# Performance work log

Hardware: AMD Instinct MI355X
Metric: run time of the kernel (lower is better)

## Reference

```python
import jax, jax.numpy as jnp
import numpy as np

PSEUDO3D = True
DO_TUBE = True
DILATION_ITERATIONS = 1

# Neighbor offsets P2..P9 (clockwise from north), as in Zhang-Suen / skimage skeletonize
_OFFS = [(-1, 0), (-1, 1), (0, 1), (1, 1), (1, 0), (1, -1), (0, -1), (-1, -1)]


def _shift(a, dy, dx):
    # out[n, y, x] = a[n, y+dy, x+dx], zero-padded borders (same as skimage's 0-pad)
    N, H, W = a.shape
    p = jnp.pad(a, ((0, 0), (1, 1), (1, 1)))
    return p[:, 1 + dy:1 + dy + H, 1 + dx:1 + dx + W]


def _subiter(img, first):
    # One Zhang-Suen sub-iteration on a stack of 2D slices [N, H, W] (bool)
    P = [_shift(img, dy, dx) for dy, dx in _OFFS]
    B = sum(p.astype(jnp.int32) for p in P)            # nonzero-neighbor count
    seq = P + [P[0]]
    A = sum(((~seq[k]) & seq[k + 1]).astype(jnp.int32) for k in range(8))  # 0->1 transitions
    P2, P3, P4, P5, P6, P7, P8, P9 = P
    if first:
        c = (~(P2 & P4 & P6)) & (~(P4 & P6 & P8))
    else:
        c = (~(P2 & P4 & P8)) & (~(P2 & P6 & P8))
    remove = img & (B >= 2) & (B <= 6) & (A == 1) & c
    return img & ~remove


def _thin_stack(stack):
    # Zhang-Suen thinning of every 2D slice in a [N, H, W] bool stack, run to convergence.
    # All slices are processed in one while_loop; converged slices are fixed points, so
    # extra iterations are no-ops and the result matches per-slice skeletonize.
    def body(state):
        img, _ = state
        new = _subiter(_subiter(img, True), False)
        return new, jnp.any(new != img)

    def cond(state):
        return state[1]

    img, _ = jax.lax.while_loop(cond, body, (stack, jnp.array(True)))
    return img


def _dilate6(v):
    # scipy.ndimage.binary_dilation with the default 6-connected 3D structure, border 0
    D, H, W = v.shape
    p = jnp.pad(v, 1)
    out = v
    for dz, dy, dx in [(1, 0, 0), (-1, 0, 0), (0, 1, 0), (0, -1, 0), (0, 0, 1), (0, 0, -1)]:
        out = out | p[1 + dz:1 + dz + D, 1 + dy:1 + dy + H, 1 + dx:1 + dx + W]
    return out


def setup_inputs() -> dict:
    key = jax.random.key(0)
    gt = jax.random.randint(key, (1, 48, 384, 384), 0, 2).astype(jnp.float32)
    return {"gt_skel": gt}


def reference(gt_skel):
    vol = gt_skel[0]                      # squeeze(axis=0) -> [D, H, W]
    mask = vol == 1.0                     # bool
    skel = _thin_stack(mask)              # per z-slice skeletonize
    if PSEUDO3D:
        # per y-slice: mask[:, y, :] has shape [D, W]
        skel = skel | jnp.transpose(_thin_stack(jnp.transpose(mask, (1, 0, 2))), (1, 0, 2))
        # per x-slice: mask[:, :, x] has shape [D, H]
        skel = skel | jnp.transpose(_thin_stack(jnp.transpose(mask, (2, 0, 1))), (1, 2, 0))
    if DO_TUBE:
        for _ in range(DILATION_ITERATIONS):
            skel = _dilate6(skel)
    skel = skel & mask                    # skel &= gt_skel.astype(bool) (values are 0/1)
    return skel[None].astype(jnp.float32)
```

## Files before the change

### kernel.cpp

```cpp
#include <hip/hip_runtime.h>

typedef unsigned long long u64;

constexpr int D = 48, H = 384, W = 384;
constexpr int WPR = 6;
constexpr int PADW = 8;
constexpr int NVOX = D * H * W;
constexpr int NWVOL = D * H * WPR;
constexpr int MPAD2 = 52;
constexpr int NXY = (D + 2) * PADW;
constexpr int NTILE = D * 36;

__device__ __forceinline__ void fa(u64 a, u64 b, u64 c, u64& s, u64& cy) {
  u64 x = a ^ b;
  s = x ^ c;
  cy = (a & b) | (c & x);
}

__device__ __forceinline__ u64 zs_regs(u64 w00, u64 w01, u64 w02,
                                       u64 w10, u64 w11, u64 w12,
                                       u64 w20, u64 w21, u64 w22, bool first) {
  const u64 P2 = w01;
  const u64 P3 = (w01 >> 1) | (w02 << 63);
  const u64 P4 = (w11 >> 1) | (w12 << 63);
  const u64 P5 = (w21 >> 1) | (w22 << 63);
  const u64 P6 = w21;
  const u64 P7 = (w21 << 1) | (w20 >> 63);
  const u64 P8 = (w11 << 1) | (w10 >> 63);
  const u64 P9 = (w01 << 1) | (w00 >> 63);

  u64 s1, c1, s2, c2, s3, c3, u0, u1, v1, v2;
  fa(P2, P3, P4, s1, c1);
  fa(P5, P6, P7, s2, c2);
  fa(P8, P9, 0ull, s3, c3);
  fa(s1, s2, s3, u0, u1);
  fa(c1, c2, c3, v1, v2);
  u64 b1 = u1 ^ v1, k2 = u1 & v1;
  u64 b2 = v2 ^ k2, b3 = v2 & k2;
  u64 condB = (b1 | b2 | b3) & ~(b3 | (b2 & b1 & u0));

  u64 t0 = ~P2 & P3, t1 = ~P3 & P4, t2 = ~P4 & P5, t3 = ~P5 & P6;
  u64 t4 = ~P6 & P7, t5 = ~P7 & P8, t6 = ~P8 & P9, t7 = ~P9 & P2;
  fa(t0, t1, t2, s1, c1);
  fa(t3, t4, t5, s2, c2);
  fa(t6, t7, 0ull, s3, c3);
  fa(s1, s2, s3, u0, u1);
  fa(c1, c2, c3, v1, v2);
  u64 a1 = u1 ^ v1, j2 = u1 & v1;
  u64 a2 = v2 ^ j2, a3 = v2 & j2;
  u64 condA = u0 & ~(a1 | a2 | a3);

  u64 cc = first ? ((~(P2 & P4 & P6)) & (~(P4 & P6 & P8)))
                 : ((~(P2 & P4 & P8)) & (~(P2 & P6 & P8)));
  return w11 & ~(condB & condA & cc);
}

__device__ __forceinline__ u64 dirty_wave(const u64* __restrict__ U, int mw) {
  const u64 A = U[mw - 1], B = U[mw], C = U[mw + 1], Dw = U[mw + 2];
  const u64 smA = A | (A >> 1 | B << 63) | (A >> 2 | B << 62);
  const u64 smB = B | (B >> 1 | C << 63) | (B >> 2 | C << 62);
  const u64 smC = C | (C >> 1 | Dw << 63) | (C >> 2 | Dw << 62);
  const u64 Dm9 = (smB << 9) | (smA >> 55);
  const u64 Dm1 = (smB << 1) | (smA >> 63);
  const u64 Dp7 = (smB >> 7) | (smC << 57);
  return Dm9 | Dm1 | Dp7;
}

template<int R, bool FIRST>
__device__ __forceinline__ void subpass(const u64* __restrict__ src, u64* __restrict__ dst,
                                        u64* rawW, const u64* rawPrev,
                                        u64* Uw, const u64* Ur,
                                        int* chgflag, int tid, int nthr) {
  constexpr int NP = (R + 2) * PADW;
  int anych = 0;
  for (int base = 0; base < NP; base += nthr) {
    const int idx = base + tid;
    int changed = 0;
    if (idx < NP) {
      const int mw = 1 + (idx >> 6);
      const u64 dmask = dirty_wave(Ur, mw);
      if ((dmask >> (idx & 63)) & 1ull) {
        const u64 old = src[idx];
        u64 nw = 0;
        if (old) {
          nw = zs_regs(src[idx - PADW - 1], src[idx - PADW], src[idx - PADW + 1],
                       src[idx - 1], old, src[idx + 1],
                       src[idx + PADW - 1], src[idx + PADW], src[idx + PADW + 1], FIRST);
          changed = (nw != old);
        }
        dst[idx] = nw;
        anych |= changed;
      }
    }
    const u64 bal = __ballot(changed != 0);
    if ((tid & 63) == 0 && idx < NP) {
      const int mw = 1 + (idx >> 6);
      rawW[mw] = bal;
      Uw[mw] = bal | rawPrev[mw];
    }
  }
  if (anych) *chgflag = 1;
}

template<bool FIRST>
__device__ __forceinline__ void xy_dense(const u64* __restrict__ src, u64* __restrict__ dst,
                                         int* chgflag, int tid) {
  int anych = 0;
  if (tid < NXY) {
    const u64 old = src[tid];
    u64 nw = 0;
    if (old) {
      nw = zs_regs(src[tid - PADW - 1], src[tid - PADW], src[tid - PADW + 1],
                   src[tid - 1], old, src[tid + 1],
                   src[tid + PADW - 1], src[tid + PADW], src[tid + PADW + 1], FIRST);
      anych = (nw != old);
    }
    dst[tid] = nw;
  }
  if (anych) *chgflag = 1;
}

template<int R>
__device__ __forceinline__ void thin_z(const u64* __restrict__ maskP,
                                       u64* __restrict__ skelZ,
                                       int slice, u64* Abuf, u64* Bbuf,
                                       u64 (*raw)[MPAD2], u64 (*Um)[MPAD2],
                                       int* s_chg) {
  constexpr int NP = (R + 2) * PADW;
  constexpr int MW = (NP + 63) >> 6;
  const int tid = threadIdx.x;
  const int nthr = 1024;

  for (int idx = tid; idx < NP; idx += nthr) {
    const int rp = idx >> 3, cp = idx & 7;
    u64 v = 0;
    if (rp >= 1 && rp <= R && cp >= 1 && cp <= 6)
      v = maskP[(slice * H + (rp - 1)) * WPR + (cp - 1)];
    Abuf[idx] = v;
    Bbuf[idx] = 0;
  }
  for (int t = tid; t < 4 * MPAD2; t += nthr) {
    const int arr = t / MPAD2, j = t - arr * MPAD2;
    const u64 v = ((arr & 1) && j >= 1 && j <= MW) ? ~0ull : 0ull;
    if (arr < 2) raw[arr][j] = v; else Um[arr - 2][j] = v;
  }
  if (tid < 2) s_chg[tid] = 0;
  __syncthreads();

  int k = 0;
  while (true) {
    subpass<R, true >(Abuf, Bbuf, raw[0], raw[1], Um[0], Um[1], &s_chg[k], tid, nthr);
    __syncthreads();
    if (tid == 0) s_chg[k ^ 1] = 0;
    subpass<R, false>(Bbuf, Abuf, raw[1], raw[0], Um[1], Um[0], &s_chg[k], tid, nthr);
    __syncthreads();
    if (s_chg[k] == 0) break;
    k ^= 1;
  }

  for (int idx = tid; idx < NP; idx += nthr) {
    const int rp = idx >> 3, cp = idx & 7;
    if (rp < 1 || rp > R || cp < 1 || cp > 6) continue;
    skelZ[(slice * H + (rp - 1)) * WPR + (cp - 1)] = Abuf[idx];
  }
}

template<int MODE>
__device__ __forceinline__ void thin_xy(const u64* __restrict__ maskP,
                                        u64* __restrict__ dstBuf,
                                        int slice, u64* Abuf, u64* Bbuf,
                                        int* s_chg) {
  const int tid = threadIdx.x;

  if (MODE == 1) {
    if (tid < NXY) {
      const int rp = tid >> 3, cp = tid & 7;
      u64 v = 0;
      if (rp >= 1 && rp <= D && cp >= 1 && cp <= 6)
        v = maskP[((rp - 1) * H + slice) * WPR + (cp - 1)];
      Abuf[tid] = v;
      Bbuf[tid] = 0;
    }
  } else {
    const int lane = tid & 63, wave = tid >> 6;
    const int xw = slice >> 6, xb = slice & 63;
    for (int w = wave; w < NXY; w += 16) {
      const int rp = w >> 3, cp = w & 7;
      u64 val = 0;
      if (rp >= 1 && rp <= D && cp >= 1 && cp <= 6) {
        const int c = (cp - 1) * 64 + lane;
        u64 bit = (maskP[((rp - 1) * H + c) * WPR + xw] >> xb) & 1ull;
        val = __ballot(bit != 0);
      }
      if (lane == 0) { Abuf[w] = val; Bbuf[w] = 0; }
    }
  }
  if (tid < 2) s_chg[tid] = 0;
  __syncthreads();

  int k = 0;
  while (true) {
    xy_dense<true >(Abuf, Bbuf, &s_chg[k], tid);
    __syncthreads();
    if (tid == 0) s_chg[k ^ 1] = 0;
    xy_dense<false>(Bbuf, Abuf, &s_chg[k], tid);
    __syncthreads();
    if (s_chg[k] == 0) break;
    k ^= 1;
  }

  if (tid < NXY) {
    const int rp = tid >> 3, cp = tid & 7;
    if (rp >= 1 && rp <= D && cp >= 1 && cp <= 6) {
      const u64 w = Abuf[tid];
      if (MODE == 1) dstBuf[((rp - 1) * H + slice) * WPR + (cp - 1)] = w;
      else           dstBuf[((rp - 1) * W + slice) * WPR + (cp - 1)] = w;
    }
  }
}

__global__ __launch_bounds__(1024) void thin_all(const u64* __restrict__ maskP,
                                                 u64* __restrict__ skelZ,
                                                 u64* __restrict__ skelY,
                                                 u64* __restrict__ skelX) {
  __shared__ u64 Abuf[(H + 2) * PADW];
  __shared__ u64 Bbuf[(H + 2) * PADW];
  __shared__ u64 raw[2][MPAD2];
  __shared__ u64 Um[2][MPAD2];
  __shared__ int s_chg[2];
  const int b = blockIdx.x;
  if (b < D) {
    thin_z<H>(maskP, skelZ, b, Abuf, Bbuf, raw, Um, s_chg);
  } else if (b < D + H) {
    thin_xy<1>(maskP, skelY, b - D, Abuf, Bbuf, s_chg);
  } else {
    thin_xy<2>(maskP, skelX, b - D - H, Abuf, Bbuf, s_chg);
  }
}

__global__ void init_pack(const float* __restrict__ in, u64* __restrict__ maskP) {
  const int lane = threadIdx.x & 63;
  const int gwave = (blockIdx.x * blockDim.x + threadIdx.x) >> 6;
  const int nwaves = (gridDim.x * blockDim.x) >> 6;
  for (int widx = gwave; widx < NWVOL; widx += nwaves) {
    float v = in[(size_t)widx * 64 + lane];
    u64 w = __ballot(v == 1.0f);
    if (lane == 0) maskP[widx] = w;
  }
}

__global__ void transpose_x(const u64* __restrict__ skelX,
                            u64* __restrict__ skelXT) {
  const int gw = (blockIdx.x * blockDim.x + threadIdx.x) >> 6;
  const int lane = threadIdx.x & 63;
  const int z = gw / 36, rem = gw - z * 36;
  const int yw = rem / 6, xw = rem - yw * 6;
  const int x = xw * 64 + lane;
  const u64 wx = skelX[(z * W + x) * WPR + yw];
  u64 mine = 0;
  #pragma unroll 8
  for (int j = 0; j < 64; ++j) {
    u64 wj = __ballot((wx >> j) & 1ull);
    if (lane == j) mine = wj;
  }
  const int y = yw * 64 + lane;
  skelXT[(z * H + y) * WPR + xw] = mine;
}

__global__ __launch_bounds__(256) void dilate_expand(const u64* __restrict__ maskP,
                                                     const u64* __restrict__ sZ,
                                                     const u64* __restrict__ sY,
                                                     const u64* __restrict__ sXT,
                                                     float* __restrict__ out) {
  __shared__ u64 rw[64];
  const int tid = threadIdx.x;
  const int wbase = blockIdx.x * 64;
  if (tid < 64) {
    const int wi = wbase + tid;
    const int wc = wi % WPR;
    const int row = wi / WPR;
    const int y = row % H;
    const int z = row / H;
    const u64 S = sZ[wi] | sY[wi] | sXT[wi];
    const u64 L = (wc > 0) ? (sZ[wi - 1] | sY[wi - 1] | sXT[wi - 1]) : 0ull;
    const u64 Rw = (wc < WPR - 1) ? (sZ[wi + 1] | sY[wi + 1] | sXT[wi + 1]) : 0ull;
    u64 d = S | (S << 1) | (L >> 63) | (S >> 1) | (Rw << 63);
    if (y > 0)     d |= sZ[wi - WPR] | sY[wi - WPR] | sXT[wi - WPR];
    if (y < H - 1) d |= sZ[wi + WPR] | sY[wi + WPR] | sXT[wi + WPR];
    if (z > 0)     d |= sZ[wi - H * WPR] | sY[wi - H * WPR] | sXT[wi - H * WPR];
    if (z < D - 1) d |= sZ[wi + H * WPR] | sY[wi + H * WPR] | sXT[wi + H * WPR];
    rw[tid] = d & maskP[wi];
  }
  __syncthreads();
  float4* o4 = reinterpret_cast<float4*>(out + (size_t)wbase * 64);
  #pragma unroll
  for (int k = 0; k < 4; ++k) {
    const int f = tid + 256 * k;
    const u64 bits = rw[f >> 4] >> ((f & 15) * 4);
    float4 o;
    o.x = (float)(bits & 1ull);
    o.y = (float)((bits >> 1) & 1ull);
    o.z = (float)((bits >> 2) & 1ull);
    o.w = (float)((bits >> 3) & 1ull);
    o4[f] = o;
  }
}

extern "C" void kernel_launch(void* const* d_in, const int* in_sizes, int n_in,
                              void* d_out, int out_size, void* d_ws, size_t ws_size,
                              hipStream_t stream) {
  const float* in = (const float*)d_in[0];
  float* out = (float*)d_out;
  u64* wsw = (u64*)d_ws;
  u64* maskP = wsw;
  u64* skelZ = wsw + NWVOL;
  u64* skelY = wsw + 2 * NWVOL;
  u64* skelX = wsw + 3 * NWVOL;
  u64* skelXT = wsw + 4 * NWVOL;

  init_pack<<<1728, 256, 0, stream>>>(in, maskP);
  thin_all<<<D + H + W, 1024, 0, stream>>>(maskP, skelZ, skelY, skelX);
  transpose_x<<<(NTILE * 64) / 256, 256, 0, stream>>>(skelX, skelXT);
  dilate_expand<<<NWVOL / 64, 256, 0, stream>>>(maskP, skelZ, skelY, skelXT, out);
}
```

Measured before the change: 61.97 us.

## Split early z-slice thinning into haloed row bands and fuse transpose

The first 16 Zhang-Suen sub-passes of each z-slice now run in four row bands per slice, each with a 16-row halo. Because one sub-pass can only change pixels one row away, the central band rows match the global result exactly. A second kernel loads that partial state per full slice and iterates to convergence, and the leftover blocks of that kernel also do the x-skeleton bit transpose, which removes a separate launch. The aim is to spread the long serial z-slice work over more blocks early on, since 48 slice blocks were likely the critical path. The cost is redundant halo computation, an extra global round trip through curZ, and the dirty-tracking masks being reset to full at the start of the finish phase.

```diff
diff --git a/kernel.cpp b/kernel.cpp
--- a/kernel.cpp
+++ b/kernel.cpp
@@ -10,6 +10,12 @@
 constexpr int MPAD2 = 52;
 constexpr int NXY = (D + 2) * PADW;
 constexpr int NTILE = D * 36;
+
+constexpr int BAND = 96;
+constexpr int HALO = 16;
+constexpr int KA = 16;
+constexpr int BROWS = BAND + 2 * HALO;
+constexpr int NBAND = H / BAND;
 
 __device__ __forceinline__ void fa(u64 a, u64 b, u64 c, u64& s, u64& cy) {
   u64 x = a ^ b;
@@ -70,10 +76,10 @@
 __device__ __forceinline__ void subpass(const u64* __restrict__ src, u64* __restrict__ dst,
                                         u64* rawW, const u64* rawPrev,
                                         u64* Uw, const u64* Ur,
-                                        int* chgflag, int tid, int nthr) {
+                                        int* chgflag, int tid) {
   constexpr int NP = (R + 2) * PADW;
   int anych = 0;
-  for (int base = 0; base < NP; base += nthr) {
+  for (int base = 0; base < NP; base += 1024) {
     const int idx = base + tid;
     int changed = 0;
     if (idx < NP) {
@@ -102,6 +108,15 @@
   if (anych) *chgflag = 1;
 }
 
+template<int MW>
+__device__ __forceinline__ void init_masks(u64 (*raw)[MPAD2], u64 (*Um)[MPAD2], int tid) {
+  for (int t = tid; t < 4 * MPAD2; t += 1024) {
+    const int arr = t / MPAD2, j = t - arr * MPAD2;
+    const u64 v = ((arr & 1) && j >= 1 && j <= MW) ? ~0ull : 0ull;
+    if (arr < 2) raw[arr][j] = v; else Um[arr - 2][j] = v;
+  }
+}
+
 template<bool FIRST>
 __device__ __forceinline__ void xy_dense(const u64* __restrict__ src, u64* __restrict__ dst,
                                          int* chgflag, int tid) {
@@ -120,48 +135,42 @@
   if (anych) *chgflag = 1;
 }
 
-template<int R>
-__device__ __forceinline__ void thin_z(const u64* __restrict__ maskP,
-                                       u64* __restrict__ skelZ,
-                                       int slice, u64* Abuf, u64* Bbuf,
-                                       u64 (*raw)[MPAD2], u64 (*Um)[MPAD2],
-                                       int* s_chg) {
-  constexpr int NP = (R + 2) * PADW;
+__device__ __forceinline__ void band_body(const u64* __restrict__ maskP,
+                                          u64* __restrict__ curZ,
+                                          int zi, int band, u64* Abuf, u64* Bbuf,
+                                          u64 (*raw)[MPAD2], u64 (*Um)[MPAD2],
+                                          int* s_chg) {
+  constexpr int NP = (BROWS + 2) * PADW;
   constexpr int MW = (NP + 63) >> 6;
   const int tid = threadIdx.x;
-  const int nthr = 1024;
-
-  for (int idx = tid; idx < NP; idx += nthr) {
+  const int g0 = band * BAND - HALO;
+
+  for (int idx = tid; idx < NP; idx += 1024) {
     const int rp = idx >> 3, cp = idx & 7;
+    const int g = g0 + rp - 1;
     u64 v = 0;
-    if (rp >= 1 && rp <= R && cp >= 1 && cp <= 6)
-      v = maskP[(slice * H + (rp - 1)) * WPR + (cp - 1)];
+    if (rp >= 1 && rp <= BROWS && cp >= 1 && cp <= 6 && g >= 0 && g < H)
+      v = maskP[(zi * H + g) * WPR + (cp - 1)];
     Abuf[idx] = v;
     Bbuf[idx] = 0;
   }
-  for (int t = tid; t < 4 * MPAD2; t += nthr) {
-    const int arr = t / MPAD2, j = t - arr * MPAD2;
-    const u64 v = ((arr & 1) && j >= 1 && j <= MW) ? ~0ull : 0ull;
-    if (arr < 2) raw[arr][j] = v; else Um[arr - 2][j] = v;
-  }
-  if (tid < 2) s_chg[tid] = 0;
+  init_masks<MW>(raw, Um, tid);
+  if (tid == 0) s_chg[0] = 0;
   __syncthreads();
 
-  int k = 0;
-  while (true) {
-    subpass<R, true >(Abuf, Bbuf, raw[0], raw[1], Um[0], Um[1], &s_chg[k], tid, nthr);
-    __syncthreads();
-    if (tid == 0) s_chg[k ^ 1] = 0;
-    subpass<R, false>(Bbuf, Abuf, raw[1], raw[0], Um[1], Um[0], &s_chg[k], tid, nthr);
-    __syncthreads();
-    if (s_chg[k] == 0) break;
-    k ^= 1;
-  }
-
-  for (int idx = tid; idx < NP; idx += nthr) {
+  for (int t = 0; t < KA; t += 2) {
+    subpass<BROWS, true >(Abuf, Bbuf, raw[0], raw[1], Um[0], Um[1], &s_chg[0], tid);
+    __syncthreads();
+    subpass<BROWS, false>(Bbuf, Abuf, raw[1], raw[0], Um[1], Um[0], &s_chg[0], tid);
+    __syncthreads();
+  }
+
+  for (int idx = tid; idx < NP; idx += 1024) {
     const int rp = idx >> 3, cp = idx & 7;
-    if (rp < 1 || rp > R || cp < 1 || cp > 6) continue;
-    skelZ[(slice * H + (rp - 1)) * WPR + (cp - 1)] = Abuf[idx];
+    if (rp < 1 || rp > BROWS || cp < 1 || cp > 6) continue;
+    const int g = g0 + rp - 1;
+    if (g < band * BAND || g >= band * BAND + BAND) continue;
+    curZ[(zi * H + g) * WPR + (cp - 1)] = Abuf[idx];
   }
 }
 
@@ -219,22 +228,85 @@
   }
 }
 
-__global__ __launch_bounds__(1024) void thin_all(const u64* __restrict__ maskP,
-                                                 u64* __restrict__ skelZ,
-                                                 u64* __restrict__ skelY,
-                                                 u64* __restrict__ skelX) {
+__global__ __launch_bounds__(1024) void thin_bands_xy(const u64* __restrict__ maskP,
+                                                      u64* __restrict__ skelY,
+                                                      u64* __restrict__ skelX,
+                                                      u64* __restrict__ curZ) {
+  __shared__ u64 Abuf[(BROWS + 2) * PADW];
+  __shared__ u64 Bbuf[(BROWS + 2) * PADW];
+  __shared__ u64 raw[2][MPAD2];
+  __shared__ u64 Um[2][MPAD2];
+  __shared__ int s_chg[2];
+  const int b = blockIdx.x;
+  if (b < D * NBAND) {
+    band_body(maskP, curZ, b >> 2, b & 3, Abuf, Bbuf, raw, Um, s_chg);
+  } else {
+    const int q = b - D * NBAND;
+    if (q < H) thin_xy<1>(maskP, skelY, q, Abuf, Bbuf, s_chg);
+    else       thin_xy<2>(maskP, skelX, q - H, Abuf, Bbuf, s_chg);
+  }
+}
+
+__global__ __launch_bounds__(1024) void thin_z_finish(const u64* __restrict__ curZ,
+                                                      u64* __restrict__ skelZ,
+                                                      const u64* __restrict__ skelX,
+                                                      u64* __restrict__ skelXT) {
   __shared__ u64 Abuf[(H + 2) * PADW];
   __shared__ u64 Bbuf[(H + 2) * PADW];
   __shared__ u64 raw[2][MPAD2];
   __shared__ u64 Um[2][MPAD2];
   __shared__ int s_chg[2];
   const int b = blockIdx.x;
+  const int tid = threadIdx.x;
+
   if (b < D) {
-    thin_z<H>(maskP, skelZ, b, Abuf, Bbuf, raw, Um, s_chg);
-  } else if (b < D + H) {
-    thin_xy<1>(maskP, skelY, b - D, Abuf, Bbuf, s_chg);
+    constexpr int NP = (H + 2) * PADW;
+    constexpr int MW = (NP + 63) >> 6;
+    for (int idx = tid; idx < NP; idx += 1024) {
+      const int rp = idx >> 3, cp = idx & 7;
+      u64 v = 0;
+      if (rp >= 1 && rp <= H && cp >= 1 && cp <= 6)
+        v = curZ[(b * H + (rp - 1)) * WPR + (cp - 1)];
+      Abuf[idx] = v;
+      Bbuf[idx] = 0;
+    }
+    init_masks<MW>(raw, Um, tid);
+    if (tid < 2) s_chg[tid] = 0;
+    __syncthreads();
+
+    int k = 0;
+    while (true) {
+      subpass<H, true >(Abuf, Bbuf, raw[0], raw[1], Um[0], Um[1], &s_chg[k], tid);
+      __syncthreads();
+      if (tid == 0) s_chg[k ^ 1] = 0;
+      subpass<H, false>(Bbuf, Abuf, raw[1], raw[0], Um[1], Um[0], &s_chg[k], tid);
+      __syncthreads();
+      if (s_chg[k] == 0) break;
+      k ^= 1;
+    }
+
+    for (int idx = tid; idx < NP; idx += 1024) {
+      const int rp = idx >> 3, cp = idx & 7;
+      if (rp < 1 || rp > H || cp < 1 || cp > 6) continue;
+      skelZ[(b * H + (rp - 1)) * WPR + (cp - 1)] = Abuf[idx];
+    }
   } else {
-    thin_xy<2>(maskP, skelX, b - D - H, Abuf, Bbuf, s_chg);
+    const int gw = (b - D) * 16 + (tid >> 6);
+    if (gw < NTILE) {
+      const int lane = tid & 63;
+      const int z = gw / 36, rem = gw - z * 36;
+      const int yw = rem / 6, xw = rem - yw * 6;
+      const int x = xw * 64 + lane;
+      const u64 wx = skelX[(z * W + x) * WPR + yw];
+      u64 mine = 0;
+      #pragma unroll 8
+      for (int j = 0; j < 64; ++j) {
+        u64 wj = __ballot((wx >> j) & 1ull);
+        if (lane == j) mine = wj;
+      }
+      const int y = yw * 64 + lane;
+      skelXT[(z * H + y) * WPR + xw] = mine;
+    }
   }
 }
 
@@ -247,24 +319,6 @@
     u64 w = __ballot(v == 1.0f);
     if (lane == 0) maskP[widx] = w;
   }
-}
-
-__global__ void transpose_x(const u64* __restrict__ skelX,
-                            u64* __restrict__ skelXT) {
-  const int gw = (blockIdx.x * blockDim.x + threadIdx.x) >> 6;
-  const int lane = threadIdx.x & 63;
-  const int z = gw / 36, rem = gw - z * 36;
-  const int yw = rem / 6, xw = rem - yw * 6;
-  const int x = xw * 64 + lane;
-  const u64 wx = skelX[(z * W + x) * WPR + yw];
-  u64 mine = 0;
-  #pragma unroll 8
-  for (int j = 0; j < 64; ++j) {
-    u64 wj = __ballot((wx >> j) & 1ull);
-    if (lane == j) mine = wj;
-  }
-  const int y = yw * 64 + lane;
-  skelXT[(z * H + y) * WPR + xw] = mine;
 }
 
 __global__ __launch_bounds__(256) void dilate_expand(const u64* __restrict__ maskP,
@@ -317,9 +371,10 @@
   u64* skelY = wsw + 2 * NWVOL;
   u64* skelX = wsw + 3 * NWVOL;
   u64* skelXT = wsw + 4 * NWVOL;
+  u64* curZ = wsw + 5 * NWVOL;
 
   init_pack<<<1728, 256, 0, stream>>>(in, maskP);
-  thin_all<<<D + H + W, 1024, 0, stream>>>(maskP, skelZ, skelY, skelX);
-  transpose_x<<<(NTILE * 64) / 256, 256, 0, stream>>>(skelX, skelXT);
+  thin_bands_xy<<<D * NBAND + H + W, 1024, 0, stream>>>(maskP, skelY, skelX, curZ);
+  thin_z_finish<<<D + (NTILE + 15) / 16, 1024, 0, stream>>>(curZ, skelZ, skelX, skelXT);
   dilate_expand<<<NWVOL / 64, 256, 0, stream>>>(maskP, skelZ, skelY, skelXT, out);
 }
```

Result: slower. 71.47 us (+15.3%).
